# Performance work log

Hardware: AMD Instinct MI355X
Metric: run time of the kernel (lower is better)

## Reference

```python
import jax, jax.numpy as jnp
import numpy as np

B, N_SLOTS, IN, MEM, OUT = 512, 128, 2048, 64, 2048


def setup_inputs() -> dict:
    key = jax.random.key(0)
    ks = jax.random.split(key, 12)

    def lin(k, fan_in, shape):
        return jax.random.normal(k, shape, dtype=jnp.float32) / np.float32(np.sqrt(fan_in))

    return {
        'x': jax.random.normal(ks[0], (B, IN), dtype=jnp.float32),
        'memory': jax.random.normal(ks[1], (B, N_SLOTS, MEM), dtype=jnp.float32),
        'W_ar': lin(ks[2], IN, (IN, MEM)),          # active_recall_net
        'b_ar': lin(ks[3], IN, (MEM,)),
        'W_pr': lin(ks[4], MEM, (MEM, 1)),          # passive_recall_net
        'b_pr': lin(ks[5], MEM, (1,)),
        'W_f': lin(ks[6], IN + MEM, (IN + MEM, 1)),  # forget_net
        'b_f': lin(ks[7], IN + MEM, (1,)),
        'W_r': lin(ks[8], IN + MEM, (IN + MEM, MEM + 1)),  # remember_net
        'b_r': lin(ks[9], IN + MEM, (MEM + 1,)),
        'W_o': lin(ks[10], IN + 2 * MEM, (IN + 2 * MEM, OUT)),  # output layer
        'b_o': lin(ks[11], IN + 2 * MEM, (OUT,)),
    }


def reference(x, memory, W_ar, b_ar, W_pr, b_pr, W_f, b_f, W_r, b_r, W_o, b_o):
    # --- active recall: score each memory slot against a projection of x ---
    q = x @ W_ar + b_ar                                   # [B, MEM]
    score = jnp.einsum('bnm,bm->bn', memory, q)           # [B, N]
    score = jax.nn.softmax(score, axis=1)[:, :, None]     # softmax over slots
    active_recall = (memory * score).sum(axis=1)          # [B, MEM]

    # --- passive recall: content-only scoring of slots ---
    p = jax.nn.softmax(memory @ W_pr + b_pr, axis=1)      # [B, N, 1]
    passive_recall = (memory * p).sum(axis=1)             # [B, MEM]

    # --- output projection ---
    intermediate = jnp.concatenate([x, active_recall, passive_recall], axis=1)
    output = intermediate @ W_o + b_o                     # [B, OUT]

    # --- gated memory update ---
    x_rep = jnp.broadcast_to(x[:, None, :], (x.shape[0], memory.shape[1], x.shape[1]))
    stack = jnp.concatenate([x_rep, memory], axis=2)      # [B, N, IN+MEM]
    forget = 1.1 * jax.nn.sigmoid(stack @ W_f + b_f)      # [B, N, 1]
    new_memory = memory * forget
    rem = stack @ W_r + b_r                               # [B, N, MEM+1]
    new_memory = new_memory + rem[:, :, -1:] * rem[:, :, :-1]
    return output, new_memory
```

## Files before the change

kernel.cpp:

```cpp
#include <hip/hip_runtime.h>
#include <hip/hip_bf16.h>


#define NB    512
#define NSLOT 128
#define DIN   2048
#define DMEM  64
#define DOUT  2048
#define PXW   130
#define KT    (DIN + 2 * DMEM)
#define NK    (KT / 32)
#define MS    72
#define OS    68

typedef __hip_bfloat16 bf16;
typedef __attribute__((ext_vector_type(8))) short short8;
typedef __attribute__((ext_vector_type(4))) float f32x4;

template<bool BF16>
__device__ __forceinline__ float ld(const void* p, size_t i) {
  if (BF16) return __bfloat162float(((const bf16*)p)[i]);
  return ((const float*)p)[i];
}
template<bool BF16>
__device__ __forceinline__ void st(void* p, size_t i, float v) {
  if (BF16) ((bf16*)p)[i] = __float2bfloat16(v);
  else      ((float*)p)[i] = v;
}
__device__ __forceinline__ unsigned short f2bu(float f) {
  unsigned int u = __builtin_bit_cast(unsigned int, f);
  u = (u + 0x7FFFu + ((u >> 16) & 1u)) >> 16;
  return (unsigned short)u;
}
__device__ __forceinline__ float bu2f(unsigned short u) {
  unsigned int w = ((unsigned int)u) << 16;
  return __builtin_bit_cast(float, w);
}

__device__ __forceinline__ bool detect_bf16(const void* x) {
  const unsigned short* u = (const unsigned short*)x;
  int lane = threadIdx.x & 63;
  unsigned short v = u[lane * 2048];
  int e = (v >> 7) & 0xFF;
  unsigned long long m = __ballot(e >= 100 && e <= 140);
  return __popcll(m) > 32;
}

union U8x16 { uint4 v; unsigned short u[8]; };

template<bool BF16>
__device__ void pack_body(
    const void* x, const void* W_ar, const void* W_pr, const void* W_f,
    const void* W_r, const void* Wo, const void* b_ar, const void* b_f,
    const void* b_r, const void* bo,
    unsigned short* Abf, unsigned short* Bt, unsigned short* Wt,
    float* bias_o, float* bias_px,
    unsigned short* Wrm, unsigned short* wprb, unsigned short* wfmb,
    unsigned short* tile) {
  int t = blockIdx.x, tid = threadIdx.x;
  if (t < 1088) {
    int kt = t % 34, nt = t / 34;
    int k0 = kt * 64, n0 = nt * 64;
    for (int i = tid; i < 64 * 64; i += 256) {
      int kk = i >> 6, nn = i & 63;
      tile[nn * 66 + kk] = f2bu(ld<BF16>(Wo, (size_t)(k0 + kk) * DOUT + n0 + nn));
    }
    __syncthreads();
    for (int i = tid; i < 64 * 64; i += 256) {
      int nn = i >> 6, kk = i & 63;
      Bt[(size_t)(n0 + nn) * KT + k0 + kk] = tile[nn * 66 + kk];
    }
  } else if (t < 1216) {
    int bx = t - 1088;
    for (int i = tid; i < 8192; i += 256) {
      int r = bx * 4 + (i >> 11), c = i & 2047;
      Abf[(size_t)r * KT + c] = f2bu(ld<BF16>(x, (size_t)r * DIN + c));
    }
  } else if (t < 1280) {
    int q = t - 1216;
    int k0 = (q >> 1) * 64, j0 = (q & 1) * 65;
    for (int i = tid; i < 64 * 65; i += 256) {
      int kl = i / 65, jl = i % 65;
      int j = j0 + jl, k = k0 + kl;
      float v;
      if (j < 64)       v = ld<BF16>(W_ar, (size_t)k * 64 + j);
      else if (j == 64) v = ld<BF16>(W_f, k);
      else              v = ld<BF16>(W_r, (size_t)k * 65 + (j - 65));
      tile[jl * 66 + kl] = f2bu(v);
    }
    __syncthreads();
    for (int i = tid; i < 65 * 64; i += 256) {
      int jl = i >> 6, kk = i & 63;
      Wt[(size_t)(j0 + jl) * DIN + k0 + kk] = tile[jl * 66 + kk];
    }
  } else if (t < 1288) {
    int c = (t - 1280) * 256 + tid;
    bias_o[c] = ld<BF16>(bo, c);
  } else if (t == 1288) {
    if (tid < PXW) {
      float v;
      if (tid < 64)       v = ld<BF16>(b_ar, tid);
      else if (tid == 64) v = ld<BF16>(b_f, 0);
      else                v = ld<BF16>(b_r, tid - 65);
      bias_px[tid] = v;
    }
  } else {
    for (int i = tid; i < 64 * 65; i += 256) {
      int k = i / 65, c = i % 65;
      tile[c * 66 + k] = f2bu(ld<BF16>(W_r, (size_t)(2048 + k) * 65 + c));
    }
    __syncthreads();
    for (int i = tid; i < 65 * 64; i += 256) {
      int c = i >> 6, k = i & 63;
      Wrm[c * 64 + k] = tile[c * 66 + k];
    }
    if (tid < 64) {
      wprb[tid] = f2bu(ld<BF16>(W_pr, tid));
      wfmb[tid] = f2bu(ld<BF16>(W_f, 2048 + tid));
    }
  }
}

__global__ __launch_bounds__(256) void k_pack(
    const void* __restrict__ x, const void* __restrict__ W_ar,
    const void* __restrict__ W_pr, const void* __restrict__ W_f,
    const void* __restrict__ W_r, const void* __restrict__ Wo,
    const void* __restrict__ b_ar, const void* __restrict__ b_f,
    const void* __restrict__ b_r, const void* __restrict__ bo,
    unsigned short* __restrict__ Abf, unsigned short* __restrict__ Bt,
    unsigned short* __restrict__ Wt, float* __restrict__ bias_o,
    float* __restrict__ bias_px, unsigned short* __restrict__ Wrm,
    unsigned short* __restrict__ wprb, unsigned short* __restrict__ wfmb) {
  __shared__ unsigned short tile[65 * 66];
  if (detect_bf16(x))
    pack_body<true >(x, W_ar, W_pr, W_f, W_r, Wo, b_ar, b_f, b_r, bo,
                     Abf, Bt, Wt, bias_o, bias_px, Wrm, wprb, wfmb, tile);
  else
    pack_body<false>(x, W_ar, W_pr, W_f, W_r, Wo, b_ar, b_f, b_r, bo,
                     Abf, Bt, Wt, bias_o, bias_px, Wrm, wprb, wfmb, tile);
}

__global__ __launch_bounds__(256) void k_proj_dot(
    const unsigned short* __restrict__ Abf,
    const unsigned short* __restrict__ Wt,
    const float* __restrict__ bias_px,
    float* __restrict__ px) {
  __shared__ float xs[DIN];
  int b = blockIdx.x;
  for (int k = threadIdx.x; k < DIN; k += 256) xs[k] = bu2f(Abf[(size_t)b * KT + k]);
  __syncthreads();
  int wv = threadIdx.x >> 6, lane = threadIdx.x & 63;
  for (int j = wv; j < PXW; j += 4) {
    const unsigned short* wc = Wt + (size_t)j * DIN;
    float acc = 0.f;
#pragma unroll
    for (int i = 0; i < 4; ++i) {
      int k0 = i * 512 + lane * 8;
      U8x16 t; t.v = *(const uint4*)(wc + k0);
      const float4* xp = (const float4*)&xs[k0];
      float4 xa = xp[0], xb = xp[1];
      acc += xa.x * bu2f(t.u[0]) + xa.y * bu2f(t.u[1])
           + xa.z * bu2f(t.u[2]) + xa.w * bu2f(t.u[3])
           + xb.x * bu2f(t.u[4]) + xb.y * bu2f(t.u[5])
           + xb.z * bu2f(t.u[6]) + xb.w * bu2f(t.u[7]);
    }
#pragma unroll
    for (int off = 32; off; off >>= 1) acc += __shfl_xor(acc, off, 64);
    if (lane == 0) px[b * PXW + j] = acc + bias_px[j];
  }
}

template<bool BF16>
__device__ void fused_body(
    const void* memory, const void* b_pr, const float* px,
    const unsigned short* Wrm, const unsigned short* wprb,
    const unsigned short* wfmb,
    unsigned short* Abf, void* dout,
    unsigned short* mem_bf, float* out_s, float* scr,
    float* sa_s, float* sp_s, float* fg_s, float* r64_s,
    float* pxr_s, float* red) {
  unsigned short* Bp = (unsigned short*)out_s;
  int b = blockIdx.x, tid = threadIdx.x;
  size_t mb = (size_t)b * (NSLOT * DMEM);

  for (int i = tid; i < NSLOT * DMEM / 2; i += 256) {
    int n = i >> 5, k2 = (i & 31) << 1;
    float v0, v1;
    if (BF16) {
      unsigned int u = ((const unsigned int*)memory)[(mb >> 1) + (size_t)i];
      v0 = bu2f((unsigned short)u); v1 = bu2f((unsigned short)(u >> 16));
    } else {
      float2 f = ((const float2*)memory)[(mb >> 1) + (size_t)i];
      v0 = f.x; v1 = f.y;
    }
    ((unsigned int*)mem_bf)[(n * MS + k2) >> 1] =
        (unsigned int)f2bu(v0) | ((unsigned int)f2bu(v1) << 16);
  }
  for (int i = tid; i < 65 * 32; i += 256) {
    int c = i >> 5, k2 = (i & 31) << 1;
    ((unsigned int*)Bp)[((3 + c) * MS + k2) >> 1] = ((const unsigned int*)Wrm)[i];
  }
  if (tid < 32) {
    int k2 = tid << 1;
    float q0 = px[b * PXW + k2], q1 = px[b * PXW + k2 + 1];
    unsigned short h0 = f2bu(q0), h1 = f2bu(q1);
    unsigned short l0 = f2bu(q0 - bu2f(h0)), l1 = f2bu(q1 - bu2f(h1));
    unsigned int* Bw = (unsigned int*)Bp;
    Bw[(0 * MS + k2) >> 1]  = (unsigned int)h0 | ((unsigned int)h1 << 16);
    Bw[(68 * MS + k2) >> 1] = (unsigned int)l0 | ((unsigned int)l1 << 16);
    Bw[(1 * MS + k2) >> 1]  = ((const unsigned int*)wprb)[tid];
    Bw[(2 * MS + k2) >> 1]  = ((const unsigned int*)wfmb)[tid];
  }
  for (int i = tid; i < 11 * 32; i += 256) {
    int c = 69 + (i >> 5), k2 = (i & 31) << 1;
    ((unsigned int*)Bp)[(c * MS + k2) >> 1] = 0;
  }
  if (tid < 65) pxr_s[tid] = px[b * PXW + 65 + tid];
  __syncthreads();

  int w = tid >> 6, lane = tid & 63;
  int lr = lane & 15, lk = (lane >> 4) * 8;
  f32x4 acc[2][5] = {};
  const unsigned short* Ab0 = &mem_bf[(w * 32 + lr) * MS + lk];
  const unsigned short* Bb  = &Bp[lr * MS + lk];
#pragma unroll
  for (int ks = 0; ks < 2; ++ks) {
    short8 a0 = *(const short8*)(Ab0 + ks * 32);
    short8 a1 = *(const short8*)(Ab0 + 16 * MS + ks * 32);
#pragma unroll
    for (int ct = 0; ct < 5; ++ct) {
      short8 bf = *(const short8*)(Bb + ct * 16 * MS + ks * 32);
      acc[0][ct] = __builtin_amdgcn_mfma_f32_16x16x32_bf16(a0, bf, acc[0][ct], 0, 0, 0);
      acc[1][ct] = __builtin_amdgcn_mfma_f32_16x16x32_bf16(a1, bf, acc[1][ct], 0, 0, 0);
    }
  }
  __syncthreads();

#pragma unroll
  for (int rt = 0; rt < 2; ++rt) {
    int row0 = w * 32 + rt * 16 + (lane >> 4) * 4;
#pragma unroll
    for (int ct = 0; ct < 5; ++ct) {
      int col = ct * 16 + lr;
#pragma unroll
      for (int r = 0; r < 4; ++r) {
        float v = acc[rt][ct][r];
        int row = row0 + r;
        if (col >= 3 && col < 67)  out_s[row * OS + (col - 3)] = v;
        else if (col == 0)         scr[0 * 128 + row] = v;
        else if (col == 68)        scr[1 * 128 + row] = v;
        else if (col == 1)         scr[2 * 128 + row] = v;
        else if (col == 2)         scr[3 * 128 + row] = v;
        else if (col == 67)        scr[4 * 128 + row] = v;
      }
    }
  }
  __syncthreads();

  float pxf = px[b * PXW + 64];
  float bpr = ld<BF16>(b_pr, 0);
  int n = tid & 127;
  float v;
  if (tid < 128) {
    v = scr[0 * 128 + n] + scr[1 * 128 + n];
    fg_s[n]  = 1.1f / (1.f + __expf(-(scr[3 * 128 + n] + pxf)));
    r64_s[n] = scr[4 * 128 + n] + pxr_s[64];
  } else {
    v = scr[2 * 128 + n] + bpr;
  }
  float mxl = v;
#pragma unroll
  for (int off = 32; off; off >>= 1) mxl = fmaxf(mxl, __shfl_xor(mxl, off, 64));
  if (lane == 0) red[w] = mxl;
  __syncthreads();
  int base = w & 2;
  float mx = fmaxf(red[base], red[base + 1]);
  float e = __expf(v - mx);
  float s = e;
#pragma unroll
  for (int off = 32; off; off >>= 1) s += __shfl_xor(s, off, 64);
  if (lane == 0) red[4 + w] = s;
  __syncthreads();
  float inv = 1.f / (red[4 + base] + red[4 + base + 1]);
  float wt = e * inv;
  if (tid < 128) sa_s[n] = wt; else sp_s[n] = wt;
  __syncthreads();

  if (tid < 128) {
    int mcol = tid & 63;
    const float* wv = (tid < 64) ? sa_s : sp_s;
    float acc2 = 0.f;
#pragma unroll 8
    for (int nn = 0; nn < NSLOT; ++nn)
      acc2 += bu2f(mem_bf[nn * MS + mcol]) * wv[nn];
    Abf[(size_t)b * KT + DIN + tid] = f2bu(acc2);
  }

  size_t obase = (size_t)NB * DOUT + mb;
  for (int i = tid; i < NSLOT * DMEM; i += 256) {
    int nn = i >> 6, j = i & 63;
    float mv  = bu2f(mem_bf[nn * MS + j]);
    float rem = out_s[nn * OS + j] + pxr_s[j];
    st<BF16>(dout, obase + i, mv * fg_s[nn] + r64_s[nn] * rem);
  }
}

__global__ __launch_bounds__(256) void k_fused(
    const void* __restrict__ x, const void* __restrict__ memory,
    const void* __restrict__ b_pr, const float* __restrict__ px,
    const unsigned short* __restrict__ Wrm,
    const unsigned short* __restrict__ wprb,
    const unsigned short* __restrict__ wfmb,
    unsigned short* __restrict__ Abf, void* __restrict__ dout) {
  __shared__ __align__(16) unsigned short mem_bf[NSLOT * MS];
  __shared__ __align__(16) float out_s[NSLOT * OS];
  __shared__ float scr[5 * 128];
  __shared__ float sa_s[128], sp_s[128], fg_s[128], r64_s[128];
  __shared__ float pxr_s[65];
  __shared__ float red[8];
  if (detect_bf16(x))
    fused_body<true >(memory, b_pr, px, Wrm, wprb, wfmb, Abf, dout,
                      mem_bf, out_s, scr, sa_s, sp_s, fg_s, r64_s, pxr_s, red);
  else
    fused_body<false>(memory, b_pr, px, Wrm, wprb, wfmb, Abf, dout,
                      mem_bf, out_s, scr, sa_s, sp_s, fg_s, r64_s, pxr_s, red);
}

template<bool BF16>
__device__ void gemm_body(const unsigned short* Abf, const unsigned short* Bt,
                          const float* bias_o, void* dout) {
  int tid = threadIdx.x;
  int lane = tid & 63, w = tid >> 6;
  int bc = blockIdx.x & 31, br = blockIdx.x >> 5;
  int col0 = bc * 64, row0 = br * 64 + w * 16;
  int lr = lane & 15, lk = (lane >> 4) * 8;

  const unsigned short* Ap = Abf + (size_t)(row0 + lr) * KT + lk;
  const unsigned short* Bp = Bt  + (size_t)(col0 + lr) * KT + lk;

  f32x4 acc0 = {}, acc1 = {}, acc2 = {}, acc3 = {};
  short8 ac  = *(const short8*)Ap;
  short8 bc0 = *(const short8*)(Bp);
  short8 bc1 = *(const short8*)(Bp + 16 * KT);
  short8 bc2 = *(const short8*)(Bp + 32 * KT);
  short8 bc3 = *(const short8*)(Bp + 48 * KT);

  for (int i = 0; i < NK; ++i) {
    short8 an = {}, bn0 = {}, bn1 = {}, bn2 = {}, bn3 = {};
    if (i + 1 < NK) {
      int k = (i + 1) * 32;
      an  = *(const short8*)(Ap + k);
      bn0 = *(const short8*)(Bp + k);
      bn1 = *(const short8*)(Bp + 16 * KT + k);
      bn2 = *(const short8*)(Bp + 32 * KT + k);
      bn3 = *(const short8*)(Bp + 48 * KT + k);
    }
    acc0 = __builtin_amdgcn_mfma_f32_16x16x32_bf16(ac, bc0, acc0, 0, 0, 0);
    acc1 = __builtin_amdgcn_mfma_f32_16x16x32_bf16(ac, bc1, acc1, 0, 0, 0);
    acc2 = __builtin_amdgcn_mfma_f32_16x16x32_bf16(ac, bc2, acc2, 0, 0, 0);
    acc3 = __builtin_amdgcn_mfma_f32_16x16x32_bf16(ac, bc3, acc3, 0, 0, 0);
    ac = an; bc0 = bn0; bc1 = bn1; bc2 = bn2; bc3 = bn3;
  }

  int rbase = row0 + (lane >> 4) * 4;
  f32x4 accs[4] = {acc0, acc1, acc2, acc3};
#pragma unroll
  for (int j = 0; j < 4; ++j) {
    int c = col0 + j * 16 + lr;
    float bias = bias_o[c];
#pragma unroll
    for (int r = 0; r < 4; ++r)
      st<BF16>(dout, (size_t)(rbase + r) * DOUT + c, accs[j][r] + bias);
  }
}

__global__ __launch_bounds__(256) void k_gemm(
    const void* __restrict__ x,
    const unsigned short* __restrict__ Abf,
    const unsigned short* __restrict__ Bt,
    const float* __restrict__ bias_o, void* __restrict__ dout) {
  if (detect_bf16(x)) gemm_body<true >(Abf, Bt, bias_o, dout);
  else                gemm_body<false>(Abf, Bt, bias_o, dout);
}

extern "C" void kernel_launch(void* const* d_in, const int* in_sizes, int n_in,
                              void* d_out, int out_size, void* d_ws, size_t ws_size,
                              hipStream_t stream) {
  const void* x    = d_in[0];
  const void* mem  = d_in[1];
  const void* W_ar = d_in[2];
  const void* b_ar = d_in[3];
  const void* W_pr = d_in[4];
  const void* b_pr = d_in[5];
  const void* W_f  = d_in[6];
  const void* b_f  = d_in[7];
  const void* W_r  = d_in[8];
  const void* b_r  = d_in[9];
  const void* W_o  = d_in[10];
  const void* b_o  = d_in[11];

  unsigned short* Abf    = (unsigned short*)d_ws;
  unsigned short* Bt     = Abf + (size_t)NB * KT;
  unsigned short* Wt     = Bt + (size_t)DOUT * KT;
  float*          bias_o = (float*)(Wt + PXW * DIN);
  float*          bias_px= bias_o + DOUT;
  float*          px     = bias_px + 132;
  unsigned short* Wrm    = (unsigned short*)(px + NB * PXW);
  unsigned short* wprb   = Wrm + 65 * 64;
  unsigned short* wfmb   = wprb + 64;

  k_pack<<<1290, 256, 0, stream>>>(x, W_ar, W_pr, W_f, W_r, W_o, b_ar, b_f,
                                   b_r, b_o, Abf, Bt, Wt, bias_o, bias_px,
                                   Wrm, wprb, wfmb);
  k_proj_dot<<<NB, 256, 0, stream>>>(Abf, Wt, bias_px, px);
  k_fused<<<NB, 256, 0, stream>>>(x, mem, b_pr, px, Wrm, wprb, wfmb, Abf, d_out);
  k_gemm<<<256, 256, 0, stream>>>(x, Abf, Bt, bias_o, d_out);
}
```

Baseline: 188.9 us.

## Use MFMA split-K for projection and LDS-staged swizzled B tiles in output GEMM

The per-batch scalar dot-product projection kernel becomes an MFMA bf16 kernel that tiles rows and columns 16x16 and splits K four ways. It writes four partial buffers, and the fused kernel sums them when it reads px. The output GEMM now stages each B tile into double-buffered shared memory through global_load_lds with an XOR swizzle, steps K by 64, and remaps block indices so neighbouring blocks share column tiles. The aim is to move the projection onto the matrix cores and to reduce redundant global B loads. The cost is more workspace, extra partial-sum reads in the fused kernel, and a barrier on every K step.

Measured after the change: 154.7 us. -18.1%, faster.

```diff
diff --git a/kernel.cpp b/kernel.cpp
--- a/kernel.cpp
+++ b/kernel.cpp
@@ -9,9 +9,10 @@
 #define DOUT  2048
 #define PXW   130
 #define KT    (DIN + 2 * DMEM)
-#define NK    (KT / 32)
 #define MS    72
 #define OS    68
+#define PXP   132
+#define PXCH  (NB * PXP)
 
 typedef __hip_bfloat16 bf16;
 typedef __attribute__((ext_vector_type(8))) short short8;
@@ -47,6 +48,17 @@
 }
 
 union U8x16 { uint4 v; unsigned short u[8]; };
+
+__device__ __forceinline__ void gload16(const void* g, void* l) {
+  __builtin_amdgcn_global_load_lds(
+      (const __attribute__((address_space(1))) unsigned int*)g,
+      (__attribute__((address_space(3))) unsigned int*)l, 16, 0, 0);
+}
+
+__device__ __forceinline__ float px4(const float* pxp, int b, int j) {
+  const float* p = pxp + (size_t)b * PXP + j;
+  return p[0] + p[PXCH] + p[2 * PXCH] + p[3 * PXCH];
+}
 
 template<bool BF16>
 __device__ void pack_body(
@@ -140,39 +152,46 @@
                      Abf, Bt, Wt, bias_o, bias_px, Wrm, wprb, wfmb, tile);
 }
 
-__global__ __launch_bounds__(256) void k_proj_dot(
+__global__ __launch_bounds__(128) void k_proj(
     const unsigned short* __restrict__ Abf,
     const unsigned short* __restrict__ Wt,
     const float* __restrict__ bias_px,
-    float* __restrict__ px) {
-  __shared__ float xs[DIN];
-  int b = blockIdx.x;
-  for (int k = threadIdx.x; k < DIN; k += 256) xs[k] = bu2f(Abf[(size_t)b * KT + k]);
-  __syncthreads();
-  int wv = threadIdx.x >> 6, lane = threadIdx.x & 63;
-  for (int j = wv; j < PXW; j += 4) {
-    const unsigned short* wc = Wt + (size_t)j * DIN;
-    float acc = 0.f;
-#pragma unroll
-    for (int i = 0; i < 4; ++i) {
-      int k0 = i * 512 + lane * 8;
-      U8x16 t; t.v = *(const uint4*)(wc + k0);
-      const float4* xp = (const float4*)&xs[k0];
-      float4 xa = xp[0], xb = xp[1];
-      acc += xa.x * bu2f(t.u[0]) + xa.y * bu2f(t.u[1])
-           + xa.z * bu2f(t.u[2]) + xa.w * bu2f(t.u[3])
-           + xb.x * bu2f(t.u[4]) + xb.y * bu2f(t.u[5])
-           + xb.z * bu2f(t.u[6]) + xb.w * bu2f(t.u[7]);
-    }
-#pragma unroll
-    for (int off = 32; off; off >>= 1) acc += __shfl_xor(acc, off, 64);
-    if (lane == 0) px[b * PXW + j] = acc + bias_px[j];
+    float* __restrict__ pxp) {
+  int wid = blockIdx.x * 2 + (threadIdx.x >> 6);
+  int lane = threadIdx.x & 63, lr = lane & 15, lk = (lane >> 4) * 8;
+  int ks = wid & 3;
+  int tt = wid >> 2;
+  int jt = tt % 9, rt = tt / 9;
+  int brow = rt * 16, j0 = jt * 16, k0 = ks * 512;
+  const unsigned short* Ap = Abf + (size_t)(brow + lr) * KT + k0 + lk;
+  const unsigned short* Bp = Wt + (size_t)(j0 + lr) * DIN + k0 + lk;
+  f32x4 acc = {};
+  short8 a0 = *(const short8*)Ap;
+  short8 b0 = *(const short8*)Bp;
+  short8 a1 = *(const short8*)(Ap + 32);
+  short8 b1 = *(const short8*)(Bp + 32);
+  for (int i = 0; i < 16; ++i) {
+    short8 a2 = {}, b2 = {};
+    if (i + 2 < 16) {
+      a2 = *(const short8*)(Ap + (i + 2) * 32);
+      b2 = *(const short8*)(Bp + (i + 2) * 32);
+    }
+    acc = __builtin_amdgcn_mfma_f32_16x16x32_bf16(a0, b0, acc, 0, 0, 0);
+    a0 = a1; b0 = b1; a1 = a2; b1 = b2;
+  }
+  int j = j0 + lr;
+  if (j < PXW) {
+    float bias = (ks == 0) ? bias_px[j] : 0.f;
+    int r0 = brow + ((lane >> 4) << 2);
+#pragma unroll
+    for (int r = 0; r < 4; ++r)
+      pxp[(size_t)ks * PXCH + (size_t)(r0 + r) * PXP + j] = acc[r] + bias;
   }
 }
 
 template<bool BF16>
 __device__ void fused_body(
-    const void* memory, const void* b_pr, const float* px,
+    const void* memory, const void* b_pr, const float* pxp,
     const unsigned short* Wrm, const unsigned short* wprb,
     const unsigned short* wfmb,
     unsigned short* Abf, void* dout,
@@ -202,7 +221,7 @@
   }
   if (tid < 32) {
     int k2 = tid << 1;
-    float q0 = px[b * PXW + k2], q1 = px[b * PXW + k2 + 1];
+    float q0 = px4(pxp, b, k2), q1 = px4(pxp, b, k2 + 1);
     unsigned short h0 = f2bu(q0), h1 = f2bu(q1);
     unsigned short l0 = f2bu(q0 - bu2f(h0)), l1 = f2bu(q1 - bu2f(h1));
     unsigned int* Bw = (unsigned int*)Bp;
@@ -215,7 +234,7 @@
     int c = 69 + (i >> 5), k2 = (i & 31) << 1;
     ((unsigned int*)Bp)[(c * MS + k2) >> 1] = 0;
   }
-  if (tid < 65) pxr_s[tid] = px[b * PXW + 65 + tid];
+  if (tid < 65) pxr_s[tid] = px4(pxp, b, 65 + tid);
   __syncthreads();
 
   int w = tid >> 6, lane = tid & 63;
@@ -257,7 +276,7 @@
   }
   __syncthreads();
 
-  float pxf = px[b * PXW + 64];
+  float pxf = px4(pxp, b, 64);
   float bpr = ld<BF16>(b_pr, 0);
   int n = tid & 127;
   float v;
@@ -307,7 +326,7 @@
 
 __global__ __launch_bounds__(256) void k_fused(
     const void* __restrict__ x, const void* __restrict__ memory,
-    const void* __restrict__ b_pr, const float* __restrict__ px,
+    const void* __restrict__ b_pr, const float* __restrict__ pxp,
     const unsigned short* __restrict__ Wrm,
     const unsigned short* __restrict__ wprb,
     const unsigned short* __restrict__ wfmb,
@@ -319,47 +338,75 @@
   __shared__ float pxr_s[65];
   __shared__ float red[8];
   if (detect_bf16(x))
-    fused_body<true >(memory, b_pr, px, Wrm, wprb, wfmb, Abf, dout,
+    fused_body<true >(memory, b_pr, pxp, Wrm, wprb, wfmb, Abf, dout,
                       mem_bf, out_s, scr, sa_s, sp_s, fg_s, r64_s, pxr_s, red);
   else
-    fused_body<false>(memory, b_pr, px, Wrm, wprb, wfmb, Abf, dout,
+    fused_body<false>(memory, b_pr, pxp, Wrm, wprb, wfmb, Abf, dout,
                       mem_bf, out_s, scr, sa_s, sp_s, fg_s, r64_s, pxr_s, red);
+}
+
+__device__ __forceinline__ void stage_b(const unsigned short* src,
+                                        unsigned short* lds,
+                                        int w, int lane) {
+#pragma unroll
+  for (int q = 0; q < 2; ++q) {
+    int c = w * 16 + q * 8 + (lane >> 3);
+    int u = lane & 7;
+    const unsigned short* gp = src + (size_t)c * KT + ((u ^ (c & 7)) << 3);
+    unsigned short* lp = lds + w * 1024 + q * 512;
+    gload16(gp, lp);
+  }
 }
 
 template<bool BF16>
 __device__ void gemm_body(const unsigned short* Abf, const unsigned short* Bt,
-                          const float* bias_o, void* dout) {
-  int tid = threadIdx.x;
-  int lane = tid & 63, w = tid >> 6;
-  int bc = blockIdx.x & 31, br = blockIdx.x >> 5;
-  int col0 = bc * 64, row0 = br * 64 + w * 16;
+                          const float* bias_o, void* dout,
+                          unsigned short (*Bs)[64 * 64]) {
+  int tid = threadIdx.x, lane = tid & 63, w = tid >> 6;
+  int bid = blockIdx.x;
+  int ct = (bid & 7) * 4 + ((bid >> 3) & 3);
+  int rt = bid >> 5;
+  int col0 = ct * 64, row0 = rt * 64 + w * 16;
   int lr = lane & 15, lk = (lane >> 4) * 8;
 
   const unsigned short* Ap = Abf + (size_t)(row0 + lr) * KT + lk;
-  const unsigned short* Bp = Bt  + (size_t)(col0 + lr) * KT + lk;
+  const unsigned short* Bg = Bt + (size_t)col0 * KT;
+
+  stage_b(Bg, &Bs[0][0], w, lane);
+  short8 a0 = *(const short8*)Ap;
+  short8 a1 = *(const short8*)(Ap + 32);
+  __syncthreads();
 
   f32x4 acc0 = {}, acc1 = {}, acc2 = {}, acc3 = {};
-  short8 ac  = *(const short8*)Ap;
-  short8 bc0 = *(const short8*)(Bp);
-  short8 bc1 = *(const short8*)(Bp + 16 * KT);
-  short8 bc2 = *(const short8*)(Bp + 32 * KT);
-  short8 bc3 = *(const short8*)(Bp + 48 * KT);
-
-  for (int i = 0; i < NK; ++i) {
-    short8 an = {}, bn0 = {}, bn1 = {}, bn2 = {}, bn3 = {};
-    if (i + 1 < NK) {
-      int k = (i + 1) * 32;
-      an  = *(const short8*)(Ap + k);
-      bn0 = *(const short8*)(Bp + k);
-      bn1 = *(const short8*)(Bp + 16 * KT + k);
-      bn2 = *(const short8*)(Bp + 32 * KT + k);
-      bn3 = *(const short8*)(Bp + 48 * KT + k);
-    }
-    acc0 = __builtin_amdgcn_mfma_f32_16x16x32_bf16(ac, bc0, acc0, 0, 0, 0);
-    acc1 = __builtin_amdgcn_mfma_f32_16x16x32_bf16(ac, bc1, acc1, 0, 0, 0);
-    acc2 = __builtin_amdgcn_mfma_f32_16x16x32_bf16(ac, bc2, acc2, 0, 0, 0);
-    acc3 = __builtin_amdgcn_mfma_f32_16x16x32_bf16(ac, bc3, acc3, 0, 0, 0);
-    ac = an; bc0 = bn0; bc1 = bn1; bc2 = bn2; bc3 = bn3;
+  int kb0 = ((lk * 2) ^ ((lr & 7) << 4)) >> 1;
+  int kb1 = ((64 + lk * 2) ^ ((lr & 7) << 4)) >> 1;
+
+  for (int i = 0; i < 34; ++i) {
+    if (i + 1 < 34) stage_b(Bg + (i + 1) * 64, &Bs[(i + 1) & 1][0], w, lane);
+    short8 an0 = {}, an1 = {};
+    if (i + 1 < 34) {
+      an0 = *(const short8*)(Ap + (i + 1) * 64);
+      an1 = *(const short8*)(Ap + (i + 1) * 64 + 32);
+    }
+    const unsigned short* bp = &Bs[i & 1][lr * 64];
+    short8 b00 = *(const short8*)(bp + 0 * 1024 + kb0);
+    short8 b01 = *(const short8*)(bp + 0 * 1024 + kb1);
+    short8 b10 = *(const short8*)(bp + 1 * 1024 + kb0);
+    short8 b11 = *(const short8*)(bp + 1 * 1024 + kb1);
+    short8 b20 = *(const short8*)(bp + 2 * 1024 + kb0);
+    short8 b21 = *(const short8*)(bp + 2 * 1024 + kb1);
+    short8 b30 = *(const short8*)(bp + 3 * 1024 + kb0);
+    short8 b31 = *(const short8*)(bp + 3 * 1024 + kb1);
+    acc0 = __builtin_amdgcn_mfma_f32_16x16x32_bf16(a0, b00, acc0, 0, 0, 0);
+    acc1 = __builtin_amdgcn_mfma_f32_16x16x32_bf16(a0, b10, acc1, 0, 0, 0);
+    acc2 = __builtin_amdgcn_mfma_f32_16x16x32_bf16(a0, b20, acc2, 0, 0, 0);
+    acc3 = __builtin_amdgcn_mfma_f32_16x16x32_bf16(a0, b30, acc3, 0, 0, 0);
+    acc0 = __builtin_amdgcn_mfma_f32_16x16x32_bf16(a1, b01, acc0, 0, 0, 0);
+    acc1 = __builtin_amdgcn_mfma_f32_16x16x32_bf16(a1, b11, acc1, 0, 0, 0);
+    acc2 = __builtin_amdgcn_mfma_f32_16x16x32_bf16(a1, b21, acc2, 0, 0, 0);
+    acc3 = __builtin_amdgcn_mfma_f32_16x16x32_bf16(a1, b31, acc3, 0, 0, 0);
+    __syncthreads();
+    a0 = an0; a1 = an1;
   }
 
   int rbase = row0 + (lane >> 4) * 4;
@@ -379,8 +426,9 @@
     const unsigned short* __restrict__ Abf,
     const unsigned short* __restrict__ Bt,
     const float* __restrict__ bias_o, void* __restrict__ dout) {
-  if (detect_bf16(x)) gemm_body<true >(Abf, Bt, bias_o, dout);
-  else                gemm_body<false>(Abf, Bt, bias_o, dout);
+  __shared__ __align__(16) unsigned short Bs[2][64 * 64];
+  if (detect_bf16(x)) gemm_body<true >(Abf, Bt, bias_o, dout, Bs);
+  else                gemm_body<false>(Abf, Bt, bias_o, dout, Bs);
 }
 
 extern "C" void kernel_launch(void* const* d_in, const int* in_sizes, int n_in,
@@ -404,15 +452,15 @@
   unsigned short* Wt     = Bt + (size_t)DOUT * KT;
   float*          bias_o = (float*)(Wt + PXW * DIN);
   float*          bias_px= bias_o + DOUT;
-  float*          px     = bias_px + 132;
-  unsigned short* Wrm    = (unsigned short*)(px + NB * PXW);
+  float*          pxp    = bias_px + 132;
+  unsigned short* Wrm    = (unsigned short*)(pxp + 4 * PXCH);
   unsigned short* wprb   = Wrm + 65 * 64;
   unsigned short* wfmb   = wprb + 64;
 
   k_pack<<<1290, 256, 0, stream>>>(x, W_ar, W_pr, W_f, W_r, W_o, b_ar, b_f,
                                    b_r, b_o, Abf, Bt, Wt, bias_o, bias_px,
                                    Wrm, wprb, wfmb);
-  k_proj_dot<<<NB, 256, 0, stream>>>(Abf, Wt, bias_px, px);
-  k_fused<<<NB, 256, 0, stream>>>(x, mem, b_pr, px, Wrm, wprb, wfmb, Abf, d_out);
+  k_proj<<<576, 128, 0, stream>>>(Abf, Wt, bias_px, pxp);
+  k_fused<<<NB, 256, 0, stream>>>(x, mem, b_pr, pxp, Wrm, wprb, wfmb, Abf, d_out);
   k_gemm<<<256, 256, 0, stream>>>(x, Abf, Bt, bias_o, d_out);
 }
```
